# Kernel optimization log

Measured on AMD Instinct MI355X. Metric: run time of the kernel, lower is better.

Reference implementation:

```python
import jax, jax.numpy as jnp
import numpy as np

DIM = 1024
NUM_HEADS = 16


def setup_inputs() -> dict:
    key = jax.random.key(0)
    ks = jax.random.split(key, 5)
    B, Nx, Ny = 8, 1024, 1024
    w_std = DIM ** -0.5  # keep logits in a sane range
    x = jax.random.normal(ks[0], (B, Nx, DIM), dtype=jnp.float32)
    y = jax.random.normal(ks[1], (B, Ny, DIM), dtype=jnp.float32)
    Wq = jax.random.normal(ks[2], (DIM, DIM), dtype=jnp.float32) * w_std
    Wk = jax.random.normal(ks[3], (DIM, DIM), dtype=jnp.float32) * w_std
    Wv = jax.random.normal(ks[4], (DIM, DIM), dtype=jnp.float32) * w_std
    return {"x": x, "y": y, "Wq": Wq, "Wk": Wk, "Wv": Wv}


def reference(x, y, Wq, Wk, Wv):
    B, Nx, dim = x.shape
    Ny = y.shape[1]
    H = NUM_HEADS
    hd = dim // H
    scale = jnp.asarray(hd ** 0.5, dtype=x.dtype)

    # torch nn.Linear: out = inp @ W.T
    Q = (x @ Wq.T) / scale                 # [B, Nx, dim]
    K = y @ Wk.T                           # [B, Ny, dim]
    V = y @ Wv.T                           # [B, Ny, dim]

    # split(last, hd) + cat(dim=0) == reshape heads to leading axis
    Qh = Q.reshape(B, Nx, H, hd)
    Kh = K.reshape(B, Ny, H, hd)
    Vh = V.reshape(B, Ny, H, hd)

    logits = jnp.einsum("bqhd,bkhd->bhqk", Qh, Kh)   # [B, H, Nx, Ny]
    A = jax.nn.softmax(logits, axis=-1)
    y_ = jnp.einsum("bhqk,bkhd->bqhd", A, Vh).reshape(B, Nx, dim)

    # second stage: x @ y_^T, scaled, softmax over queries (dim=-2)
    s = jnp.einsum("bqd,bkd->bqk", x, y_) / scale    # [B, Nx, Nx]
    return jax.nn.softmax(s, axis=-2)
```

## Files before the change

kernel.cpp:

```cpp
#include <hip/hip_runtime.h>

typedef unsigned short ushort_t;
typedef __attribute__((ext_vector_type(8))) short short8;
typedef __attribute__((ext_vector_type(4))) float f32x4;
typedef __attribute__((ext_vector_type(2))) unsigned uint2v;

#define DIM 1024
#define BATCH 8
#define NSEQ 1024
#define HEADS 16
#define HD 64

__device__ __forceinline__ ushort_t f2b(float f) {
    union { float f; unsigned u; } v; v.f = f;
    unsigned r = v.u + 0x7FFF + ((v.u >> 16) & 1);
    return (ushort_t)(r >> 16);
}

__device__ __forceinline__ unsigned cvtpk_bf16(float a, float b) {
    unsigned r;
    asm("v_cvt_pk_bf16_f32 %0, %1, %2" : "=v"(r) : "v"(a), "v"(b));
    return r;
}

__device__ __forceinline__ void g2l16(const void* g, void* l) {
    __builtin_amdgcn_global_load_lds(
        (const __attribute__((address_space(1))) void*)g,
        (__attribute__((address_space(3))) void*)l, 16, 0, 0);
}

__global__ __launch_bounds__(256) void conv_bf16(const float4* __restrict__ src,
                                                 short8* __restrict__ dst) {
    int i = blockIdx.x * 256 + threadIdx.x;
    float4 a = src[i * 2], b = src[i * 2 + 1];
    short8 o;
    o[0] = (short)f2b(a.x); o[1] = (short)f2b(a.y);
    o[2] = (short)f2b(a.z); o[3] = (short)f2b(a.w);
    o[4] = (short)f2b(b.x); o[5] = (short)f2b(b.y);
    o[6] = (short)f2b(b.z); o[7] = (short)f2b(b.w);
    dst[i] = o;
}

template <typename OutT, int MODE>
__global__ __launch_bounds__(256) void gemm_nt(const ushort_t* __restrict__ A,
                                               const ushort_t* __restrict__ B,
                                               OutT* __restrict__ C,
                                               long sA, long sB, long sC,
                                               float scale) {
    __shared__ __align__(16) ushort_t As[128 * 64];
    __shared__ __align__(16) ushort_t Bs[128 * 64];
    const int tid = threadIdx.x;
    const int w = tid >> 6, l = tid & 63;
    const int wm = w >> 1, wn = w & 1;
    const int lo = l & 15, hi = l >> 4;

    int bx, by, bz;
    const int j = blockIdx.x;
    if constexpr (MODE == 1) { by = j & 63; bx = j >> 6; bz = 0; }
    else if constexpr (MODE == 2) { bx = j & 7; by = (j >> 3) & 7; bz = j >> 6; }
    else { bz = j & 7; bx = (j >> 3) & 7; by = j >> 6; }

    const long abase = (long)by * 128 * 1024 + (long)bz * sA;
    const long bbase = (long)bx * 128 * 1024 + (long)bz * sB;
    const char* Abytes = (const char*)A;
    const char* Bbytes = (const char*)B;

    f32x4 acc[4][4];
#pragma unroll
    for (int m = 0; m < 4; m++)
#pragma unroll
        for (int n = 0; n < 4; n++) acc[m][n] = (f32x4)0.f;

    for (int kt = 0; kt < 1024; kt += 64) {
#pragma unroll
        for (int i = 0; i < 4; i++) {
            int o16 = tid + i * 256;
            int row = o16 >> 3;
            int cb = (o16 & 7) * 16;
            int scb = cb ^ ((row & 7) << 4);
            g2l16(Abytes + (abase + (long)row * 1024 + kt) * 2 + scb,
                  (char*)As + o16 * 16);
            g2l16(Bbytes + (bbase + (long)row * 1024 + kt) * 2 + scb,
                  (char*)Bs + o16 * 16);
        }
        __syncthreads();
#pragma unroll
        for (int kc = 0; kc < 2; kc++) {
            short8 af[4], bfr[4];
#pragma unroll
            for (int m = 0; m < 4; m++) {
                int row = wm * 64 + m * 16 + lo;
                int cb = (kc * 64 + hi * 16) ^ ((row & 7) << 4);
                af[m] = *(const short8*)((const char*)As + row * 128 + cb);
            }
#pragma unroll
            for (int n = 0; n < 4; n++) {
                int row = wn * 64 + n * 16 + lo;
                int cb = (kc * 64 + hi * 16) ^ ((row & 7) << 4);
                bfr[n] = *(const short8*)((const char*)Bs + row * 128 + cb);
            }
            __builtin_amdgcn_s_setprio(1);
#pragma unroll
            for (int m = 0; m < 4; m++)
#pragma unroll
                for (int n = 0; n < 4; n++)
                    acc[m][n] = __builtin_amdgcn_mfma_f32_16x16x32_bf16(
                        af[m], bfr[n], acc[m][n], 0, 0, 0);
            __builtin_amdgcn_s_setprio(0);
        }
        __syncthreads();
    }

    const long cb0 = (long)bz * sC;
#pragma unroll
    for (int m = 0; m < 4; m++)
#pragma unroll
        for (int n = 0; n < 4; n++)
#pragma unroll
            for (int r = 0; r < 4; r++) {
                long row = (long)by * 128 + wm * 64 + m * 16 + hi * 4 + r;
                long col = (long)bx * 128 + wn * 64 + n * 16 + lo;
                float v = acc[m][n][r] * scale;
                if constexpr (sizeof(OutT) == 2)
                    C[cb0 + row * 1024 + col] = (OutT)f2b(v);
                else
                    C[cb0 + row * 1024 + col] = v;
            }
}

__global__ __launch_bounds__(256, 4) void flash_attn(const ushort_t* __restrict__ Q,
                                                     const ushort_t* __restrict__ Kb,
                                                     const ushort_t* __restrict__ Vt,
                                                     ushort_t* __restrict__ Yo) {
    __shared__ __align__(16) ushort_t Ks[2][64 * 64];
    __shared__ __align__(16) ushort_t Vs[2][64 * 64];
    __shared__ __align__(16) unsigned Ps[4][32 * 16];
    const int j = blockIdx.x;
    const int g = j & 127, qt = j >> 7;
    const int h = g & 15, b = g >> 4;
    const int tid = threadIdx.x, w = tid >> 6, l = tid & 63;
    const int lo = l & 15, hi = l >> 4;
    const int sw = (lo & 7) << 4;
    const int psw = (lo >> 1) & 3;

    const char* Khb = (const char*)(Kb + (long)b * 1024 * 1024 + h * 64);
    const char* Vhb = (const char*)(Vt + (long)b * 1024 * 1024 + (long)h * 64 * 1024);

    const long qrow0 = (long)b * 1024 + qt * 128 + w * 32;
    short8 qf[2][2];
#pragma unroll
    for (int qg = 0; qg < 2; qg++)
#pragma unroll
        for (int dk = 0; dk < 2; dk++)
            qf[qg][dk] = *(const short8*)(Q + (qrow0 + qg * 16 + lo) * 1024 +
                                          h * 64 + dk * 32 + hi * 8);

    float m_prev[2] = {-1e30f, -1e30f}, l_sum[2] = {0.f, 0.f};
    f32x4 o_acc[4][2];
#pragma unroll
    for (int ch = 0; ch < 4; ch++)
#pragma unroll
        for (int qg = 0; qg < 2; qg++) o_acc[ch][qg] = (f32x4)0.f;

    {
#pragma unroll
        for (int i = 0; i < 2; i++) {
            int o16 = tid + i * 256;
            int row = o16 >> 3, cb = (o16 & 7) * 16;
            int scb = cb ^ ((row & 7) << 4);
            g2l16(Khb + (long)row * 2048 + scb, (char*)Ks[0] + o16 * 16);
            g2l16(Vhb + (long)row * 2048 + scb, (char*)Vs[0] + o16 * 16);
        }
    }

    unsigned* Pw = Ps[w];

    for (int t = 0; t < 16; t++) {
        __syncthreads();
        if (t < 15) {
            int kt = (t + 1) * 64;
            int bufn = (t + 1) & 1;
#pragma unroll
            for (int i = 0; i < 2; i++) {
                int o16 = tid + i * 256;
                int row = o16 >> 3, cb = (o16 & 7) * 16;
                int scb = cb ^ ((row & 7) << 4);
                g2l16(Khb + ((long)(kt + row) * 1024) * 2 + scb,
                      (char*)Ks[bufn] + o16 * 16);
                g2l16(Vhb + ((long)row * 1024 + kt) * 2 + scb,
                      (char*)Vs[bufn] + o16 * 16);
            }
        }
        const char* Kc = (const char*)Ks[t & 1];
        const char* Vc = (const char*)Vs[t & 1];

        f32x4 s_acc[4][2];
        __builtin_amdgcn_s_setprio(1);
#pragma unroll
        for (int ks = 0; ks < 4; ks++) {
            const char* kr = Kc + (ks * 16 + lo) * 128;
            short8 kf0 = *(const short8*)(kr + ((hi * 16) ^ sw));
            short8 kf1 = *(const short8*)(kr + ((64 + hi * 16) ^ sw));
#pragma unroll
            for (int qg = 0; qg < 2; qg++) {
                s_acc[ks][qg] = __builtin_amdgcn_mfma_f32_16x16x32_bf16(
                    kf0, qf[qg][0], (f32x4)0.f, 0, 0, 0);
                s_acc[ks][qg] = __builtin_amdgcn_mfma_f32_16x16x32_bf16(
                    kf1, qf[qg][1], s_acc[ks][qg], 0, 0, 0);
            }
        }
        __builtin_amdgcn_s_setprio(0);

        float mt[2];
#pragma unroll
        for (int qg = 0; qg < 2; qg++) {
            float m0 = s_acc[0][qg][0];
#pragma unroll
            for (int ks = 0; ks < 4; ks++)
#pragma unroll
                for (int r = 0; r < 4; r++)
                    if (ks | r) m0 = fmaxf(m0, s_acc[ks][qg][r]);
            m0 = fmaxf(m0, __shfl_xor(m0, 16));
            m0 = fmaxf(m0, __shfl_xor(m0, 32));
            mt[qg] = m0;
        }

        if (__any((mt[0] > m_prev[0] + 8.f) || (mt[1] > m_prev[1] + 8.f))) {
            float corr[2];
#pragma unroll
            for (int qg = 0; qg < 2; qg++) {
                float mn = fmaxf(m_prev[qg], mt[qg]);
                corr[qg] = exp2f(m_prev[qg] - mn);
                m_prev[qg] = mn;
                l_sum[qg] *= corr[qg];
            }
#pragma unroll
            for (int qg = 0; qg < 2; qg++)
#pragma unroll
                for (int r = 0; r < 4; r++) {
                    float c = __shfl(corr[qg], hi * 4 + r);
#pragma unroll
                    for (int ch = 0; ch < 4; ch++) o_acc[ch][qg][r] *= c;
                }
        }

#pragma unroll
        for (int qg = 0; qg < 2; qg++) {
            float ps = 0.f;
#pragma unroll
            for (int ks = 0; ks < 4; ks++)
#pragma unroll
                for (int r = 0; r < 4; r++) {
                    float p = exp2f(s_acc[ks][qg][r] - m_prev[qg]);
                    s_acc[ks][qg][r] = p;
                    ps += p;
                }
            ps += __shfl_xor(ps, 16);
            ps += __shfl_xor(ps, 32);
            l_sum[qg] += ps;
        }

#pragma unroll
        for (int kk = 0; kk < 2; kk++) {
#pragma unroll
            for (int qg = 0; qg < 2; qg++)
#pragma unroll
                for (int ksh = 0; ksh < 2; ksh++) {
                    int slot = ksh * 2 + (hi >> 1);
                    int u = ((qg * 16 + lo) << 4) | ((slot ^ psw) << 2) | ((hi & 1) << 1);
                    uint2v v2;
                    v2[0] = cvtpk_bf16(s_acc[kk * 2 + ksh][qg][0], s_acc[kk * 2 + ksh][qg][1]);
                    v2[1] = cvtpk_bf16(s_acc[kk * 2 + ksh][qg][2], s_acc[kk * 2 + ksh][qg][3]);
                    *(uint2v*)(Pw + u) = v2;
                }
            __builtin_amdgcn_wave_barrier();
            short8 pa[2];
#pragma unroll
            for (int qg = 0; qg < 2; qg++)
                pa[qg] = *(const short8*)(Pw + (((qg * 16 + lo) << 4) | ((hi ^ psw) << 2)));
            __builtin_amdgcn_s_setprio(1);
#pragma unroll
            for (int ch = 0; ch < 4; ch++) {
                short8 vf = *(const short8*)(Vc + (ch * 16 + lo) * 128 +
                                             ((kk * 64 + hi * 16) ^ sw));
#pragma unroll
                for (int qg = 0; qg < 2; qg++)
                    o_acc[ch][qg] = __builtin_amdgcn_mfma_f32_16x16x32_bf16(
                        pa[qg], vf, o_acc[ch][qg], 0, 0, 0);
            }
            __builtin_amdgcn_s_setprio(0);
            __builtin_amdgcn_wave_barrier();
        }
    }

    float inv[2][4];
#pragma unroll
    for (int qg = 0; qg < 2; qg++)
#pragma unroll
        for (int r = 0; r < 4; r++)
            inv[qg][r] = 1.f / __shfl(l_sum[qg], hi * 4 + r);
#pragma unroll
    for (int ch = 0; ch < 4; ch++)
#pragma unroll
        for (int qg = 0; qg < 2; qg++)
#pragma unroll
            for (int r = 0; r < 4; r++) {
                long row = qrow0 + qg * 16 + hi * 4 + r;
                Yo[row * 1024 + h * 64 + ch * 16 + lo] =
                    f2b(o_acc[ch][qg][r] * inv[qg][r]);
            }
}

__global__ __launch_bounds__(256) void col_softmax(float* __restrict__ S) {
    const int b = blockIdx.y;
    const int colbase = blockIdx.x * 32;
    const int c = threadIdx.x & 31, g = threadIdx.x >> 5;
    float* p = S + (long)b * 1024 * 1024 + colbase + c;
    float m = -1e30f, s = 0.f;
    for (int r = 0; r < 128; r++) {
        float v = p[(long)(g * 128 + r) * 1024];
        float mn = fmaxf(m, v);
        s = s * __expf(m - mn) + __expf(v - mn);
        m = mn;
    }
    __shared__ float pm[8][32], ps[8][32];
    pm[g][c] = m; ps[g][c] = s;
    __syncthreads();
    float M = -1e30f;
#pragma unroll
    for (int gg = 0; gg < 8; gg++) M = fmaxf(M, pm[gg][c]);
    float Ssum = 0.f;
#pragma unroll
    for (int gg = 0; gg < 8; gg++) Ssum += ps[gg][c] * __expf(pm[gg][c] - M);
    float inv = 1.f / Ssum;
    for (int r = 0; r < 128; r++) {
        long idx = (long)(g * 128 + r) * 1024;
        p[idx] = __expf(p[idx] - M) * inv;
    }
}

extern "C" void kernel_launch(void* const* d_in, const int* in_sizes, int n_in,
                              void* d_out, int out_size, void* d_ws, size_t ws_size,
                              hipStream_t stream) {
    const float* x = (const float*)d_in[0];
    const float* y = (const float*)d_in[1];
    const float* Wq = (const float*)d_in[2];
    const float* Wk = (const float*)d_in[3];
    const float* Wv = (const float*)d_in[4];
    float* out = (float*)d_out;

    const long NXD = (long)BATCH * NSEQ * DIM;
    const long WSZ = (long)DIM * DIM;
    ushort_t* xb = (ushort_t*)d_ws;
    ushort_t* yb = xb + NXD;
    ushort_t* wqb = yb + NXD;
    ushort_t* wkb = wqb + WSZ;
    ushort_t* wvb = wkb + WSZ;
    ushort_t* Qb = wvb + WSZ;
    ushort_t* Kbb = Qb + NXD;
    ushort_t* Vtb = Kbb + NXD;
    ushort_t* Yob = Vtb + NXD;

    conv_bf16<<<NXD / 2048, 256, 0, stream>>>((const float4*)x, (short8*)xb);
    conv_bf16<<<NXD / 2048, 256, 0, stream>>>((const float4*)y, (short8*)yb);
    conv_bf16<<<WSZ / 2048, 256, 0, stream>>>((const float4*)Wq, (short8*)wqb);
    conv_bf16<<<WSZ / 2048, 256, 0, stream>>>((const float4*)Wk, (short8*)wkb);
    conv_bf16<<<WSZ / 2048, 256, 0, stream>>>((const float4*)Wv, (short8*)wvb);

    gemm_nt<ushort_t, 1><<<512, 256, 0, stream>>>(xb, wqb, Qb, 0, 0, 0,
                                                  0.125f * 1.44269504f);
    gemm_nt<ushort_t, 1><<<512, 256, 0, stream>>>(yb, wkb, Kbb, 0, 0, 0, 1.0f);
    gemm_nt<ushort_t, 2><<<512, 256, 0, stream>>>(wvb, yb, Vtb, 0, WSZ, WSZ, 1.0f);
    flash_attn<<<1024, 256, 0, stream>>>(Qb, Kbb, Vtb, Yob);
    gemm_nt<float, 3><<<512, 256, 0, stream>>>(xb, Yob, out, WSZ, WSZ, WSZ, 0.125f);
    col_softmax<<<dim3(32, 8), 256, 0, stream>>>(out);
}
```

Baseline: 302.6 us.

## Transpose P in registers via permlane swaps and merge conversion launches

The flash-attention kernel no longer round-trips the softmax probabilities through a per-wave LDS buffer to rearrange them into the MFMA A-operand layout. It does the rearrangement in registers with permlane32/permlane16 swap instructions, which removes the LDS stores, loads and wave barriers and frees that shared memory. The max and sum reductions are rewritten as trees to shorten dependency chains. The five fp32-to-bf16 conversion launches are merged into one kernel that picks its source by block index, cutting launch overhead. The permlane lane mapping must exactly match the layout the old LDS path produced, or the results will be wrong.

```diff
diff --git a/kernel.cpp b/kernel.cpp
--- a/kernel.cpp
+++ b/kernel.cpp
@@ -4,6 +4,7 @@
 typedef __attribute__((ext_vector_type(8))) short short8;
 typedef __attribute__((ext_vector_type(4))) float f32x4;
 typedef __attribute__((ext_vector_type(2))) unsigned uint2v;
+typedef __attribute__((ext_vector_type(4))) unsigned uint4v;
 
 #define DIM 1024
 #define BATCH 8
@@ -29,9 +30,24 @@
         (__attribute__((address_space(3))) void*)l, 16, 0, 0);
 }
 
-__global__ __launch_bounds__(256) void conv_bf16(const float4* __restrict__ src,
-                                                 short8* __restrict__ dst) {
-    int i = blockIdx.x * 256 + threadIdx.x;
+__global__ __launch_bounds__(256) void conv_all(const float4* __restrict__ x,
+                                                const float4* __restrict__ y,
+                                                const float4* __restrict__ wq,
+                                                const float4* __restrict__ wk,
+                                                const float4* __restrict__ wv,
+                                                short8* __restrict__ xb,
+                                                short8* __restrict__ yb,
+                                                short8* __restrict__ wqb,
+                                                short8* __restrict__ wkb,
+                                                short8* __restrict__ wvb) {
+    int j = blockIdx.x;
+    const float4* src; short8* dst; int base;
+    if (j < 4096)      { src = x;  dst = xb;  base = j; }
+    else if (j < 8192) { src = y;  dst = yb;  base = j - 4096; }
+    else if (j < 8704) { src = wq; dst = wqb; base = j - 8192; }
+    else if (j < 9216) { src = wk; dst = wkb; base = j - 8704; }
+    else               { src = wv; dst = wvb; base = j - 9216; }
+    int i = base * 256 + threadIdx.x;
     float4 a = src[i * 2], b = src[i * 2 + 1];
     short8 o;
     o[0] = (short)f2b(a.x); o[1] = (short)f2b(a.y);
@@ -134,14 +150,12 @@
                                                      ushort_t* __restrict__ Yo) {
     __shared__ __align__(16) ushort_t Ks[2][64 * 64];
     __shared__ __align__(16) ushort_t Vs[2][64 * 64];
-    __shared__ __align__(16) unsigned Ps[4][32 * 16];
     const int j = blockIdx.x;
     const int g = j & 127, qt = j >> 7;
     const int h = g & 15, b = g >> 4;
     const int tid = threadIdx.x, w = tid >> 6, l = tid & 63;
     const int lo = l & 15, hi = l >> 4;
     const int sw = (lo & 7) << 4;
-    const int psw = (lo >> 1) & 3;
 
     const char* Khb = (const char*)(Kb + (long)b * 1024 * 1024 + h * 64);
     const char* Vhb = (const char*)(Vt + (long)b * 1024 * 1024 + (long)h * 64 * 1024);
@@ -172,8 +186,6 @@
             g2l16(Vhb + (long)row * 2048 + scb, (char*)Vs[0] + o16 * 16);
         }
     }
-
-    unsigned* Pw = Ps[w];
 
     for (int t = 0; t < 16; t++) {
         __syncthreads();
@@ -214,12 +226,13 @@
         float mt[2];
 #pragma unroll
         for (int qg = 0; qg < 2; qg++) {
-            float m0 = s_acc[0][qg][0];
+            float mk[4];
 #pragma unroll
             for (int ks = 0; ks < 4; ks++)
-#pragma unroll
-                for (int r = 0; r < 4; r++)
-                    if (ks | r) m0 = fmaxf(m0, s_acc[ks][qg][r]);
+                mk[ks] = fmaxf(fmaxf(fmaxf(s_acc[ks][qg][0], s_acc[ks][qg][1]),
+                                     s_acc[ks][qg][2]),
+                               s_acc[ks][qg][3]);
+            float m0 = fmaxf(fmaxf(fmaxf(mk[0], mk[1]), mk[2]), mk[3]);
             m0 = fmaxf(m0, __shfl_xor(m0, 16));
             m0 = fmaxf(m0, __shfl_xor(m0, 32));
             mt[qg] = m0;
@@ -244,17 +257,21 @@
                 }
         }
 
+        unsigned pk[2][4][2];
 #pragma unroll
         for (int qg = 0; qg < 2; qg++) {
-            float ps = 0.f;
-#pragma unroll
-            for (int ks = 0; ks < 4; ks++)
-#pragma unroll
-                for (int r = 0; r < 4; r++) {
-                    float p = exp2f(s_acc[ks][qg][r] - m_prev[qg]);
-                    s_acc[ks][qg][r] = p;
-                    ps += p;
-                }
+            float psk[4];
+#pragma unroll
+            for (int ks = 0; ks < 4; ks++) {
+#pragma unroll
+                for (int r = 0; r < 4; r++)
+                    s_acc[ks][qg][r] = exp2f(s_acc[ks][qg][r] - m_prev[qg]);
+                psk[ks] = (s_acc[ks][qg][0] + s_acc[ks][qg][1]) +
+                          (s_acc[ks][qg][2] + s_acc[ks][qg][3]);
+                pk[qg][ks][0] = cvtpk_bf16(s_acc[ks][qg][0], s_acc[ks][qg][1]);
+                pk[qg][ks][1] = cvtpk_bf16(s_acc[ks][qg][2], s_acc[ks][qg][3]);
+            }
+            float ps = (psk[0] + psk[1]) + (psk[2] + psk[3]);
             ps += __shfl_xor(ps, 16);
             ps += __shfl_xor(ps, 32);
             l_sum[qg] += ps;
@@ -262,22 +279,19 @@
 
 #pragma unroll
         for (int kk = 0; kk < 2; kk++) {
-#pragma unroll
-            for (int qg = 0; qg < 2; qg++)
-#pragma unroll
-                for (int ksh = 0; ksh < 2; ksh++) {
-                    int slot = ksh * 2 + (hi >> 1);
-                    int u = ((qg * 16 + lo) << 4) | ((slot ^ psw) << 2) | ((hi & 1) << 1);
-                    uint2v v2;
-                    v2[0] = cvtpk_bf16(s_acc[kk * 2 + ksh][qg][0], s_acc[kk * 2 + ksh][qg][1]);
-                    v2[1] = cvtpk_bf16(s_acc[kk * 2 + ksh][qg][2], s_acc[kk * 2 + ksh][qg][3]);
-                    *(uint2v*)(Pw + u) = v2;
-                }
-            __builtin_amdgcn_wave_barrier();
             short8 pa[2];
 #pragma unroll
-            for (int qg = 0; qg < 2; qg++)
-                pa[qg] = *(const short8*)(Pw + (((qg * 16 + lo) << 4) | ((hi ^ psw) << 2)));
+            for (int qg = 0; qg < 2; qg++) {
+                unsigned a0 = pk[qg][2 * kk][0], b0 = pk[qg][2 * kk + 1][0];
+                uint2v t0 = __builtin_amdgcn_permlane32_swap(a0, b0, false, false);
+                t0 = __builtin_amdgcn_permlane16_swap(t0[0], t0[1], false, false);
+                unsigned a1 = pk[qg][2 * kk][1], b1 = pk[qg][2 * kk + 1][1];
+                uint2v t1 = __builtin_amdgcn_permlane32_swap(a1, b1, false, false);
+                t1 = __builtin_amdgcn_permlane16_swap(t1[0], t1[1], false, false);
+                union { uint4v u; short8 s; } cv;
+                cv.u = (uint4v){t0[0], t1[0], t0[1], t1[1]};
+                pa[qg] = cv.s;
+            }
             __builtin_amdgcn_s_setprio(1);
 #pragma unroll
             for (int ch = 0; ch < 4; ch++) {
@@ -289,7 +303,6 @@
                         pa[qg], vf, o_acc[ch][qg], 0, 0, 0);
             }
             __builtin_amdgcn_s_setprio(0);
-            __builtin_amdgcn_wave_barrier();
         }
     }
 
@@ -361,11 +374,10 @@
     ushort_t* Vtb = Kbb + NXD;
     ushort_t* Yob = Vtb + NXD;
 
-    conv_bf16<<<NXD / 2048, 256, 0, stream>>>((const float4*)x, (short8*)xb);
-    conv_bf16<<<NXD / 2048, 256, 0, stream>>>((const float4*)y, (short8*)yb);
-    conv_bf16<<<WSZ / 2048, 256, 0, stream>>>((const float4*)Wq, (short8*)wqb);
-    conv_bf16<<<WSZ / 2048, 256, 0, stream>>>((const float4*)Wk, (short8*)wkb);
-    conv_bf16<<<WSZ / 2048, 256, 0, stream>>>((const float4*)Wv, (short8*)wvb);
+    conv_all<<<9728, 256, 0, stream>>>((const float4*)x, (const float4*)y,
+                                       (const float4*)Wq, (const float4*)Wk,
+                                       (const float4*)Wv, (short8*)xb, (short8*)yb,
+                                       (short8*)wqb, (short8*)wkb, (short8*)wvb);
 
     gemm_nt<ushort_t, 1><<<512, 256, 0, stream>>>(xb, wqb, Qb, 0, 0, 0,
                                                   0.125f * 1.44269504f);
```

Measured after the change: 299.2 us. Within noise of the previous version (-1.1%).
